# Performance work log

Measured on AMD Instinct MI355X. Metric: run time of the kernel, lower is better.

## Reference

```python
import jax, jax.numpy as jnp
import numpy as np
import math

D = 1024
H = 16
B = 4
N = 2048


def setup_inputs() -> dict:
    key = jax.random.key(0)
    ks = jax.random.split(key, 10)
    scale_qkv = 0.01
    def kaiming_uniform(k, shape, scale):
        # attenuated_kaiming_uniform_: fan_in = shape[1], gain for leaky_relu a=sqrt(5)
        fan_in = shape[1]
        gain = math.sqrt(2.0 / (1 + 5.0))
        bound = math.sqrt(3.0) * gain * scale / math.sqrt(fan_in)
        return jax.random.uniform(k, shape, jnp.float32, -bound, bound)
    return {
        "x_q": jax.random.normal(ks[0], (B, N, D), jnp.float32),
        "x_kv": jax.random.normal(ks[1], (B, N, D), jnp.float32),
        "Wq": kaiming_uniform(ks[2], (D, D), scale_qkv),
        "bq": jnp.zeros((D,), jnp.float32),
        "Wk": kaiming_uniform(ks[3], (D, D), scale_qkv),
        "bk": jnp.zeros((D,), jnp.float32),
        "Wv": kaiming_uniform(ks[4], (D, D), scale_qkv),
        "bv": jnp.zeros((D,), jnp.float32),
        "Wo": kaiming_uniform(ks[5], (D, D), 1.0),
        "bo": jnp.zeros((D,), jnp.float32),
    }


def reference(x_q, x_kv, Wq, bq, Wk, bk, Wv, bv, Wo, bo):
    bs, n, d = x_q.shape
    hd = d // H  # head dim
    # torch Linear: y = x @ W^T + b
    q = x_q @ Wq.T + bq
    k = x_kv @ Wk.T + bk
    v = x_kv @ Wv.T + bv
    # reshape to [bs, H, n, hd]
    q = q.reshape(bs, n, H, hd).transpose(0, 2, 1, 3)
    k = k.reshape(bs, n, H, hd).transpose(0, 2, 1, 3)
    v = v.reshape(bs, n, H, hd).transpose(0, 2, 1, 3)
    scores = jnp.einsum("bhqd,bhkd->bhqk", q, k) / math.sqrt(hd)
    seq_ids = jnp.arange(n)
    causal = (seq_ids[None, :] <= seq_ids[:, None]).astype(scores.dtype)  # [n, n]
    scores = scores + (1.0 - causal) * -10000.0
    probs = jax.nn.softmax(scores, axis=-1)
    out = jnp.einsum("bhqk,bhkd->bhqd", probs, v)
    out = out.transpose(0, 2, 1, 3).reshape(bs, n, d)
    return out @ Wo.T + bo
```

## Files before the change

kernel.cpp:

```cpp
#include <hip/hip_runtime.h>

typedef unsigned short u16;
typedef unsigned int u32;
typedef __attribute__((ext_vector_type(8))) short short8;
typedef __attribute__((ext_vector_type(4))) float f32x4;

#define ASYNC_CP16(gsrc, ldst) \
  __builtin_amdgcn_global_load_lds((__attribute__((address_space(1))) void*)(gsrc), \
                                   (__attribute__((address_space(3))) void*)(ldst), 16, 0, 0)

static __device__ __forceinline__ u16 f2bf(float f) {
  u32 u = __builtin_bit_cast(u32, f);
  u = u + 0x7fffu + ((u >> 16) & 1u);
  return (u16)(u >> 16);
}
static __device__ __forceinline__ u32 pk2(float a, float b) {
  return (u32)f2bf(a) | ((u32)f2bf(b) << 16);
}
static __device__ __forceinline__ u32 pk2r(float a, float b) {
  u32 ua = __builtin_bit_cast(u32, a) + 0x8000u;
  u32 ub = __builtin_bit_cast(u32, b) + 0x8000u;
  return __builtin_amdgcn_perm(ub, ua, 0x07060302);
}

__global__ __launch_bounds__(256) void convert_all(
    const float* __restrict__ xq, const float* __restrict__ xkv,
    const float* __restrict__ wq, const float* __restrict__ wk,
    const float* __restrict__ wv, const float* __restrict__ wo,
    u16* __restrict__ dst)
{
  long i = ((long)blockIdx.x * 256 + threadIdx.x) * 4;
  const float* s; long o;
  if      (i < 8388608)  { s = xq;  o = i; }
  else if (i < 16777216) { s = xkv; o = i - 8388608; }
  else if (i < 17825792) { s = wq;  o = i - 16777216; }
  else if (i < 18874368) { s = wk;  o = i - 17825792; }
  else if (i < 19922944) { s = wv;  o = i - 18874368; }
  else                   { s = wo;  o = i - 19922944; }
  float4 v = *(const float4*)(s + o);
  uint2 pkv; pkv.x = pk2(v.x, v.y); pkv.y = pk2(v.z, v.w);
  *(uint2*)(dst + i) = pkv;
}

template<int EPI>
__global__ __launch_bounds__(256)
void gemm_k(const u16* __restrict__ Axq, const u16* __restrict__ Axkv,
            const u16* __restrict__ W0, const u16* __restrict__ W1, const u16* __restrict__ W2,
            const float* __restrict__ b0, const float* __restrict__ b1, const float* __restrict__ b2,
            u16* __restrict__ Qo, u16* __restrict__ Ko, u16* __restrict__ Vo,
            float* __restrict__ Fo)
{
  __shared__ u16 lsa[128*32];
  __shared__ u16 lsb[128*32];
  const int tid = threadIdx.x;
  const int w = tid >> 6, lane = tid & 63;
  const int wr = w >> 1, wc = w & 1;
  const int bm = blockIdx.x, bn = blockIdx.y, z = blockIdx.z;
  const int l15 = lane & 15, l4 = lane >> 4;

  const u16* A; const u16* W; const float* bias;
  if (EPI == 0) {
    A    = (z == 0) ? Axq : Axkv;
    W    = (z == 0) ? W0 : (z == 1) ? W1 : W2;
    bias = (z == 0) ? b0 : (z == 1) ? b1 : b2;
  } else {
    A = Axq; W = W0; bias = b0;
  }
  const u16* Ag = A + (long)bm*128*1024;
  const u16* Wg = W + (long)bn*128*1024;

  f32x4 acc[4][4];
#pragma unroll
  for (int i = 0; i < 4; ++i)
#pragma unroll
    for (int j = 0; j < 4; ++j)
      acc[i][j] = (f32x4){0.f,0.f,0.f,0.f};

  for (int k0 = 0; k0 < 1024; k0 += 32) {
    __syncthreads();
#pragma unroll
    for (int c = 0; c < 2; ++c) {
      int tp = c*256 + tid;
      int row = tp >> 2, col = (tp & 3) * 8;
      ASYNC_CP16(Ag + (long)row*1024 + k0 + col, &lsa[tp*8]);
      ASYNC_CP16(Wg + (long)row*1024 + k0 + col, &lsb[tp*8]);
    }
    __syncthreads();
    short8 af[4], bfr[4];
#pragma unroll
    for (int i = 0; i < 4; ++i)
      af[i] = *(const short8*)&lsa[(wr*64 + i*16 + l15)*32 + l4*8];
#pragma unroll
    for (int j = 0; j < 4; ++j)
      bfr[j] = *(const short8*)&lsb[(wc*64 + j*16 + l15)*32 + l4*8];
#pragma unroll
    for (int i = 0; i < 4; ++i)
#pragma unroll
      for (int j = 0; j < 4; ++j)
        acc[i][j] = __builtin_amdgcn_mfma_f32_16x16x32_bf16(af[i], bfr[j], acc[i][j], 0, 0, 0);
  }

#pragma unroll
  for (int j = 0; j < 4; ++j) {
    const int colg = bn*128 + wc*64 + j*16 + l15;
    const float bb = bias[colg];
#pragma unroll
    for (int i = 0; i < 4; ++i) {
      const int rowg = bm*128 + wr*64 + i*16 + l4*4;
      if (EPI == 1) {
#pragma unroll
        for (int r = 0; r < 4; ++r)
          Fo[(long)(rowg + r)*1024 + colg] = acc[i][j][r] + bb;
      } else {
        const int b  = rowg >> 11, n0 = rowg & 2047;
        const int h  = colg >> 6,  c  = colg & 63;
        const int bh = b*16 + h;
        const long hb = (long)bh*131072 + (long)(n0 >> 7)*8192;
        if (z == 0) {
#pragma unroll
          for (int r = 0; r < 4; ++r)
            Qo[((long)bh*2048 + n0 + r)*64 + c] = f2bf((acc[i][j][r] + bb) * 0.18033688f);
        } else if (z == 1) {
          const long base = hb + (long)(c >> 3)*1024 + (n0 & 127)*8 + (c & 7);
#pragma unroll
          for (int r = 0; r < 4; ++r)
            Ko[base + r*8] = f2bf(acc[i][j][r] + bb);
        } else {
          const long base = hb + (long)((n0 & 127) >> 3)*512 + (long)c*8 + (n0 & 7);
          uint2 pkv;
          pkv.x = pk2(acc[i][j][0] + bb, acc[i][j][1] + bb);
          pkv.y = pk2(acc[i][j][2] + bb, acc[i][j][3] + bb);
          *(uint2*)(Vo + base) = pkv;
        }
      }
    }
  }
}

__global__ __launch_bounds__(256)
void attn_k(const u16* __restrict__ Q, const u16* __restrict__ K,
            const u16* __restrict__ V, u16* __restrict__ AO)
{
  __shared__ u16 lk[8192];
  __shared__ u16 lv[8192];
  __shared__ u16 lp[4][1024];
  const int tid = threadIdx.x;
  const int w = tid >> 6, lane = tid & 63;
  const int l15 = lane & 15, l4 = lane >> 4;
  const int qt = (gridDim.x - 1) - blockIdx.x;
  const int bh = blockIdx.y;
  const int q0 = qt*64;
  const int qg = q0 + w*16 + l15;
  const u16* Qh = Q + (long)bh*131072;
  const u16* Kh = K + (long)bh*131072;
  const u16* Vh = V + (long)bh*131072;

  short8 qf[2];
#pragma unroll
  for (int ks = 0; ks < 2; ++ks)
    qf[ks] = *(const short8*)&Qh[(long)qg*64 + ks*32 + l4*8];

  f32x4 o[4];
#pragma unroll
  for (int nt = 0; nt < 4; ++nt) o[nt] = (f32x4){0.f,0.f,0.f,0.f};
  float rsum = 0.f;

  u16* pw = &lp[w][0];
  const int swz_q = (l15 & 7);
  const int ktmax = (q0 + 63) >> 7;
  for (int kt = 0; kt <= ktmax; ++kt) {
    __syncthreads();
#pragma unroll
    for (int c = 0; c < 4; ++c) {
      int tp = c*256 + tid;
      ASYNC_CP16(Kh + (long)kt*8192 + tp*8, &lk[tp*8]);
      ASYNC_CP16(Vh + (long)kt*8192 + tp*8, &lv[tp*8]);
    }
    __syncthreads();

    f32x4 s[8];
#pragma unroll
    for (int nt = 0; nt < 8; ++nt) s[nt] = (f32x4){0.f,0.f,0.f,0.f};
#pragma unroll
    for (int ks = 0; ks < 2; ++ks)
#pragma unroll
      for (int nt = 0; nt < 8; ++nt) {
        short8 kf = *(const short8*)&lk[(ks*4 + l4)*1024 + (nt*16 + l15)*8];
        s[nt] = __builtin_amdgcn_mfma_f32_16x16x32_bf16(kf, qf[ks], s[nt], 0, 0, 0);
      }

    if (kt*128 + 127 > q0) {
      const int kb = kt*128 + l4*4;
#pragma unroll
      for (int nt = 0; nt < 8; ++nt)
#pragma unroll
        for (int r = 0; r < 4; ++r)
          if (kb + nt*16 + r > qg) s[nt][r] = -1e30f;
    }

    u32 pk[8][2];
#pragma unroll
    for (int nt = 0; nt < 8; ++nt) {
      float p0 = __builtin_amdgcn_exp2f(s[nt][0]);
      float p1 = __builtin_amdgcn_exp2f(s[nt][1]);
      float p2 = __builtin_amdgcn_exp2f(s[nt][2]);
      float p3 = __builtin_amdgcn_exp2f(s[nt][3]);
      rsum += (p0 + p1) + (p2 + p3);
      pk[nt][0] = pk2r(p0, p1);
      pk[nt][1] = pk2r(p2, p3);
    }

#pragma unroll
    for (int h = 0; h < 2; ++h) {
#pragma unroll
      for (int ntl = 0; ntl < 4; ++ntl) {
        const int chunk = ntl*2 + (l4 >> 1);
        const int swz = chunk ^ swz_q;
        uint2 pr; pr.x = pk[4*h + ntl][0]; pr.y = pk[4*h + ntl][1];
        *(uint2*)&pw[l15*64 + swz*8 + (l4 & 1)*4] = pr;
      }
#pragma unroll
      for (int ksl = 0; ksl < 2; ++ksl) {
        const int swz = (ksl*4 + l4) ^ swz_q;
        short8 pf = *(const short8*)&pw[l15*64 + swz*8];
        const int ksg = h*2 + ksl;
#pragma unroll
        for (int nt = 0; nt < 4; ++nt) {
          short8 vf = *(const short8*)&lv[(ksg*4 + l4)*512 + (nt*16 + l15)*8];
          o[nt] = __builtin_amdgcn_mfma_f32_16x16x32_bf16(vf, pf, o[nt], 0, 0, 0);
        }
      }
    }
  }

  rsum += __shfl_xor(rsum, 16, 64);
  rsum += __shfl_xor(rsum, 32, 64);

  const int b = bh >> 4, h = bh & 15;
  const float inv = 1.0f / rsum;
  const long tok = (long)b*2048 + qg;
#pragma unroll
  for (int nt = 0; nt < 4; ++nt) {
    uint2 pkv;
    pkv.x = pk2(o[nt][0]*inv, o[nt][1]*inv);
    pkv.y = pk2(o[nt][2]*inv, o[nt][3]*inv);
    *(uint2*)&AO[tok*1024 + h*64 + nt*16 + l4*4] = pkv;
  }
}

extern "C" void kernel_launch(void* const* d_in, const int* in_sizes, int n_in,
                              void* d_out, int out_size, void* d_ws, size_t ws_size,
                              hipStream_t stream)
{
  const float* xq  = (const float*)d_in[0];
  const float* xkv = (const float*)d_in[1];
  const float* Wq  = (const float*)d_in[2];
  const float* bq  = (const float*)d_in[3];
  const float* Wk  = (const float*)d_in[4];
  const float* bk  = (const float*)d_in[5];
  const float* Wv  = (const float*)d_in[6];
  const float* bv  = (const float*)d_in[7];
  const float* Wo  = (const float*)d_in[8];
  const float* bo  = (const float*)d_in[9];

  u16* ws    = (u16*)d_ws;
  u16* xq_b  = ws;
  u16* xkv_b = xq_b  + (1l<<23);
  u16* wq_b  = xkv_b + (1l<<23);
  u16* wk_b  = wq_b  + (1l<<20);
  u16* wv_b  = wk_b  + (1l<<20);
  u16* wo_b  = wv_b  + (1l<<20);
  u16* Qb    = wo_b  + (1l<<20);
  u16* Kb    = Qb    + (1l<<23);
  u16* Vb    = Kb    + (1l<<23);
  u16* Ab    = Vb    + (1l<<23);

  convert_all<<<20480, 256, 0, stream>>>(xq, xkv, Wq, Wk, Wv, Wo, ws);
  gemm_k<0><<<dim3(64,8,3), 256, 0, stream>>>(xq_b, xkv_b, wq_b, wk_b, wv_b,
                                              bq, bk, bv, Qb, Kb, Vb, nullptr);
  attn_k<<<dim3(32,64), 256, 0, stream>>>(Qb, Kb, Vb, Ab);
  gemm_k<1><<<dim3(64,8,1), 256, 0, stream>>>(Ab, nullptr, wo_b, nullptr, nullptr,
                                              bo, nullptr, nullptr,
                                              nullptr, nullptr, nullptr,
                                              (float*)d_out);
}
```

Baseline: 344.1 us.

## Enlarge attention query tiles, keep P in registers, skip masked diagonal tiles

The attention kernel now processes 128 queries per block (32 per wave, two 16-row groups), so each K/V tile loaded into LDS is reused twice as much and the grid halves. The P matrix no longer round-trips through LDS: exp values stay in registers and feed 16x16x16 bf16 MFMAs with V as the A operand, which needs a new swizzled V layout written by the projection GEMM. The last (diagonal) tile is specialised to skip fully masked sub-tiles. The GEMM epilogue swaps operands for Q/K/output so stores become vectorised along the feature dimension. The cost is more registers per wave, and it relies on the MFMA16 builtin choice being correct.

Result: slower. 406.4 us (+18.1%).

```diff
diff --git a/kernel.cpp b/kernel.cpp
--- a/kernel.cpp
+++ b/kernel.cpp
@@ -3,11 +3,24 @@
 typedef unsigned short u16;
 typedef unsigned int u32;
 typedef __attribute__((ext_vector_type(8))) short short8;
+typedef __attribute__((ext_vector_type(4))) short s16x4;
 typedef __attribute__((ext_vector_type(4))) float f32x4;
 
 #define ASYNC_CP16(gsrc, ldst) \
   __builtin_amdgcn_global_load_lds((__attribute__((address_space(1))) void*)(gsrc), \
                                    (__attribute__((address_space(3))) void*)(ldst), 16, 0, 0)
+
+#if __has_builtin(__builtin_amdgcn_mfma_f32_16x16x16bf16_1k)
+#define MFMA16(A, B, C) __builtin_amdgcn_mfma_f32_16x16x16bf16_1k(A, B, C, 0, 0, 0)
+#elif __has_builtin(__builtin_amdgcn_mfma_f32_16x16x16_bf16)
+#define MFMA16(A, B, C) __builtin_amdgcn_mfma_f32_16x16x16_bf16(A, B, C, 0, 0, 0)
+#else
+static __device__ __forceinline__ f32x4 mfma16_asm(s16x4 a, s16x4 b, f32x4 c) {
+  asm("v_mfma_f32_16x16x16_bf16 %0, %1, %2, %0" : "+v"(c) : "v"(a), "v"(b));
+  return c;
+}
+#define MFMA16(A, B, C) mfma16_asm(A, B, C)
+#endif
 
 static __device__ __forceinline__ u16 f2bf(float f) {
   u32 u = __builtin_bit_cast(u32, f);
@@ -69,6 +82,10 @@
   const u16* Ag = A + (long)bm*128*1024;
   const u16* Wg = W + (long)bn*128*1024;
 
+  const bool swapop = (EPI == 1) || (z != 2);
+  const u16* pAs = swapop ? lsb : lsa;
+  const u16* pBs = swapop ? lsa : lsb;
+
   f32x4 acc[4][4];
 #pragma unroll
   for (int i = 0; i < 4; ++i)
@@ -89,10 +106,10 @@
     short8 af[4], bfr[4];
 #pragma unroll
     for (int i = 0; i < 4; ++i)
-      af[i] = *(const short8*)&lsa[(wr*64 + i*16 + l15)*32 + l4*8];
+      af[i] = *(const short8*)&pAs[(wr*64 + i*16 + l15)*32 + l4*8];
 #pragma unroll
     for (int j = 0; j < 4; ++j)
-      bfr[j] = *(const short8*)&lsb[(wc*64 + j*16 + l15)*32 + l4*8];
+      bfr[j] = *(const short8*)&pBs[(wc*64 + j*16 + l15)*32 + l4*8];
 #pragma unroll
     for (int i = 0; i < 4; ++i)
 #pragma unroll
@@ -100,37 +117,122 @@
         acc[i][j] = __builtin_amdgcn_mfma_f32_16x16x32_bf16(af[i], bfr[j], acc[i][j], 0, 0, 0);
   }
 
-#pragma unroll
-  for (int j = 0; j < 4; ++j) {
-    const int colg = bn*128 + wc*64 + j*16 + l15;
-    const float bb = bias[colg];
+  if (swapop) {
 #pragma unroll
     for (int i = 0; i < 4; ++i) {
-      const int rowg = bm*128 + wr*64 + i*16 + l4*4;
-      if (EPI == 1) {
-#pragma unroll
-        for (int r = 0; r < 4; ++r)
-          Fo[(long)(rowg + r)*1024 + colg] = acc[i][j][r] + bb;
-      } else {
-        const int b  = rowg >> 11, n0 = rowg & 2047;
-        const int h  = colg >> 6,  c  = colg & 63;
-        const int bh = b*16 + h;
-        const long hb = (long)bh*131072 + (long)(n0 >> 7)*8192;
-        if (z == 0) {
-#pragma unroll
-          for (int r = 0; r < 4; ++r)
-            Qo[((long)bh*2048 + n0 + r)*64 + c] = f2bf((acc[i][j][r] + bb) * 0.18033688f);
-        } else if (z == 1) {
-          const long base = hb + (long)(c >> 3)*1024 + (n0 & 127)*8 + (c & 7);
-#pragma unroll
-          for (int r = 0; r < 4; ++r)
-            Ko[base + r*8] = f2bf(acc[i][j][r] + bb);
+      const int dg = bn*128 + wr*64 + i*16 + l4*4;
+      const float4 b4 = *(const float4*)&bias[dg];
+#pragma unroll
+      for (int j = 0; j < 4; ++j) {
+        const int tk = bm*128 + wc*64 + j*16 + l15;
+        const float v0 = acc[i][j][0] + b4.x, v1 = acc[i][j][1] + b4.y;
+        const float v2 = acc[i][j][2] + b4.z, v3 = acc[i][j][3] + b4.w;
+        if (EPI == 1) {
+          *(float4*)&Fo[(long)tk*1024 + dg] = (float4){v0, v1, v2, v3};
+        } else if (z == 0) {
+          const int bb_ = tk >> 11, n = tk & 2047, h = dg >> 6, c0 = dg & 63;
+          uint2 pv;
+          pv.x = pk2(v0*0.18033688f, v1*0.18033688f);
+          pv.y = pk2(v2*0.18033688f, v3*0.18033688f);
+          *(uint2*)&Qo[((long)(bb_*16 + h)*2048 + n)*64 + c0] = pv;
         } else {
-          const long base = hb + (long)((n0 & 127) >> 3)*512 + (long)c*8 + (n0 & 7);
-          uint2 pkv;
-          pkv.x = pk2(acc[i][j][0] + bb, acc[i][j][1] + bb);
-          pkv.y = pk2(acc[i][j][2] + bb, acc[i][j][3] + bb);
-          *(uint2*)(Vo + base) = pkv;
+          const int bb_ = tk >> 11, n = tk & 2047, h = dg >> 6, d0 = dg & 63;
+          const long base = (long)(bb_*16 + h)*131072 + (long)(n >> 7)*8192
+                          + (d0 >> 3)*1024 + (n & 127)*8 + (d0 & 7);
+          uint2 pv; pv.x = pk2(v0, v1); pv.y = pk2(v2, v3);
+          *(uint2*)&Ko[base] = pv;
+        }
+      }
+    }
+  } else {
+#pragma unroll
+    for (int j = 0; j < 4; ++j) {
+      const int colg = bn*128 + wc*64 + j*16 + l15;
+      const float bb = bias[colg];
+      const int h = colg >> 6, c = colg & 63;
+#pragma unroll
+      for (int i = 0; i < 4; ++i) {
+        const int rowg = bm*128 + wr*64 + i*16 + l4*4;
+        const int bb_ = rowg >> 11, n0 = rowg & 2047;
+        const long base = (long)(bb_*16 + h)*131072 + (long)(n0 >> 7)*8192
+                        + ((n0 & 127) >> 5)*2048 + (long)c*32
+                        + ((n0 >> 4) & 1)*4 + ((((n0 >> 2) & 3) ^ ((c >> 1) & 3)))*8;
+        uint2 pv;
+        pv.x = pk2(acc[i][j][0] + bb, acc[i][j][1] + bb);
+        pv.y = pk2(acc[i][j][2] + bb, acc[i][j][3] + bb);
+        *(uint2*)&Vo[base] = pv;
+      }
+    }
+  }
+}
+
+template<bool LAST>
+static __device__ __forceinline__ void attn_step(
+    const u16* __restrict__ Kh, const u16* __restrict__ Vh, long kt,
+    u16* lk, u16* lv, int tid, int w, int l4, int l15,
+    const short8 (&qf)[2][2], f32x4 (&o)[2][4], float (&rs)[2])
+{
+  __syncthreads();
+#pragma unroll
+  for (int c2 = 0; c2 < 4; ++c2) {
+    int tp = c2*256 + tid;
+    ASYNC_CP16(Kh + kt*8192 + tp*8, &lk[tp*8]);
+    ASYNC_CP16(Vh + kt*8192 + tp*8, &lv[tp*8]);
+  }
+  __syncthreads();
+
+  s16x4 pkv[2][8];
+#pragma unroll
+  for (int c = 0; c < 2; ++c) {
+    const int ntl = 2*w + c;
+    f32x4 s[8];
+#pragma unroll
+    for (int nt = 0; nt < 8; ++nt) {
+      if (!LAST || nt <= ntl) {
+        f32x4 a = (f32x4){0.f,0.f,0.f,0.f};
+#pragma unroll
+        for (int ks = 0; ks < 2; ++ks) {
+          short8 kf = *(const short8*)&lk[(ks*4 + l4)*1024 + (nt*16 + l15)*8];
+          a = __builtin_amdgcn_mfma_f32_16x16x32_bf16(kf, qf[c][ks], a, 0, 0, 0);
+        }
+        s[nt] = a;
+      }
+    }
+    if (LAST) {
+#pragma unroll
+      for (int r = 0; r < 4; ++r)
+        if (l4*4 + r > l15) s[ntl][r] = -1e30f;
+    }
+#pragma unroll
+    for (int nt = 0; nt < 8; ++nt) {
+      if (!LAST || nt <= ntl) {
+        float p0 = __builtin_amdgcn_exp2f(s[nt][0]);
+        float p1 = __builtin_amdgcn_exp2f(s[nt][1]);
+        float p2 = __builtin_amdgcn_exp2f(s[nt][2]);
+        float p3 = __builtin_amdgcn_exp2f(s[nt][3]);
+        rs[c] += (p0 + p1) + (p2 + p3);
+        union { uint2 u; s16x4 v; } pu;
+        pu.u.x = pk2r(p0, p1);
+        pu.u.y = pk2r(p2, p3);
+        pkv[c][nt] = pu.v;
+      }
+    }
+  }
+
+  const int swz = l4 ^ ((l15 >> 1) & 3);
+#pragma unroll
+  for (int g = 0; g < 4; ++g) {
+    if (!LAST || 2*g <= 2*w + 1) {
+#pragma unroll
+      for (int ntd = 0; ntd < 4; ++ntd) {
+        short8 vv = *(const short8*)&lv[g*2048 + (ntd*16 + l15)*32 + swz*8];
+        s16x4 v0 = __builtin_shufflevector(vv, vv, 0, 1, 2, 3);
+        s16x4 v1 = __builtin_shufflevector(vv, vv, 4, 5, 6, 7);
+#pragma unroll
+        for (int c = 0; c < 2; ++c) {
+          const int ntl = 2*w + c;
+          if (!LAST || 2*g <= ntl)     o[c][ntd] = MFMA16(v0, pkv[c][2*g],     o[c][ntd]);
+          if (!LAST || 2*g + 1 <= ntl) o[c][ntd] = MFMA16(v1, pkv[c][2*g + 1], o[c][ntd]);
         }
       }
     }
@@ -143,108 +245,49 @@
 {
   __shared__ u16 lk[8192];
   __shared__ u16 lv[8192];
-  __shared__ u16 lp[4][1024];
   const int tid = threadIdx.x;
   const int w = tid >> 6, lane = tid & 63;
   const int l15 = lane & 15, l4 = lane >> 4;
-  const int qt = (gridDim.x - 1) - blockIdx.x;
+  const int qt = 15 - blockIdx.x;
   const int bh = blockIdx.y;
-  const int q0 = qt*64;
-  const int qg = q0 + w*16 + l15;
+  const int q0 = qt*128, qbase = q0 + w*32;
   const u16* Qh = Q + (long)bh*131072;
   const u16* Kh = K + (long)bh*131072;
   const u16* Vh = V + (long)bh*131072;
 
-  short8 qf[2];
-#pragma unroll
-  for (int ks = 0; ks < 2; ++ks)
-    qf[ks] = *(const short8*)&Qh[(long)qg*64 + ks*32 + l4*8];
-
-  f32x4 o[4];
-#pragma unroll
-  for (int nt = 0; nt < 4; ++nt) o[nt] = (f32x4){0.f,0.f,0.f,0.f};
-  float rsum = 0.f;
-
-  u16* pw = &lp[w][0];
-  const int swz_q = (l15 & 7);
-  const int ktmax = (q0 + 63) >> 7;
-  for (int kt = 0; kt <= ktmax; ++kt) {
-    __syncthreads();
-#pragma unroll
-    for (int c = 0; c < 4; ++c) {
-      int tp = c*256 + tid;
-      ASYNC_CP16(Kh + (long)kt*8192 + tp*8, &lk[tp*8]);
-      ASYNC_CP16(Vh + (long)kt*8192 + tp*8, &lv[tp*8]);
-    }
-    __syncthreads();
-
-    f32x4 s[8];
-#pragma unroll
-    for (int nt = 0; nt < 8; ++nt) s[nt] = (f32x4){0.f,0.f,0.f,0.f};
+  short8 qf[2][2];
+#pragma unroll
+  for (int c = 0; c < 2; ++c)
 #pragma unroll
     for (int ks = 0; ks < 2; ++ks)
-#pragma unroll
-      for (int nt = 0; nt < 8; ++nt) {
-        short8 kf = *(const short8*)&lk[(ks*4 + l4)*1024 + (nt*16 + l15)*8];
-        s[nt] = __builtin_amdgcn_mfma_f32_16x16x32_bf16(kf, qf[ks], s[nt], 0, 0, 0);
-      }
-
-    if (kt*128 + 127 > q0) {
-      const int kb = kt*128 + l4*4;
-#pragma unroll
-      for (int nt = 0; nt < 8; ++nt)
-#pragma unroll
-        for (int r = 0; r < 4; ++r)
-          if (kb + nt*16 + r > qg) s[nt][r] = -1e30f;
-    }
-
-    u32 pk[8][2];
-#pragma unroll
-    for (int nt = 0; nt < 8; ++nt) {
-      float p0 = __builtin_amdgcn_exp2f(s[nt][0]);
-      float p1 = __builtin_amdgcn_exp2f(s[nt][1]);
-      float p2 = __builtin_amdgcn_exp2f(s[nt][2]);
-      float p3 = __builtin_amdgcn_exp2f(s[nt][3]);
-      rsum += (p0 + p1) + (p2 + p3);
-      pk[nt][0] = pk2r(p0, p1);
-      pk[nt][1] = pk2r(p2, p3);
-    }
-
-#pragma unroll
-    for (int h = 0; h < 2; ++h) {
-#pragma unroll
-      for (int ntl = 0; ntl < 4; ++ntl) {
-        const int chunk = ntl*2 + (l4 >> 1);
-        const int swz = chunk ^ swz_q;
-        uint2 pr; pr.x = pk[4*h + ntl][0]; pr.y = pk[4*h + ntl][1];
-        *(uint2*)&pw[l15*64 + swz*8 + (l4 & 1)*4] = pr;
-      }
-#pragma unroll
-      for (int ksl = 0; ksl < 2; ++ksl) {
-        const int swz = (ksl*4 + l4) ^ swz_q;
-        short8 pf = *(const short8*)&pw[l15*64 + swz*8];
-        const int ksg = h*2 + ksl;
-#pragma unroll
-        for (int nt = 0; nt < 4; ++nt) {
-          short8 vf = *(const short8*)&lv[(ksg*4 + l4)*512 + (nt*16 + l15)*8];
-          o[nt] = __builtin_amdgcn_mfma_f32_16x16x32_bf16(vf, pf, o[nt], 0, 0, 0);
-        }
-      }
-    }
-  }
-
-  rsum += __shfl_xor(rsum, 16, 64);
-  rsum += __shfl_xor(rsum, 32, 64);
+      qf[c][ks] = *(const short8*)&Qh[(long)(qbase + c*16 + l15)*64 + ks*32 + l4*8];
+
+  f32x4 o[2][4];
+#pragma unroll
+  for (int c = 0; c < 2; ++c)
+#pragma unroll
+    for (int nt = 0; nt < 4; ++nt) o[c][nt] = (f32x4){0.f,0.f,0.f,0.f};
+  float rs[2] = {0.f, 0.f};
+
+  for (int kt = 0; kt < qt; ++kt)
+    attn_step<false>(Kh, Vh, kt, lk, lv, tid, w, l4, l15, qf, o, rs);
+  attn_step<true>(Kh, Vh, qt, lk, lv, tid, w, l4, l15, qf, o, rs);
 
   const int b = bh >> 4, h = bh & 15;
-  const float inv = 1.0f / rsum;
-  const long tok = (long)b*2048 + qg;
-#pragma unroll
-  for (int nt = 0; nt < 4; ++nt) {
-    uint2 pkv;
-    pkv.x = pk2(o[nt][0]*inv, o[nt][1]*inv);
-    pkv.y = pk2(o[nt][2]*inv, o[nt][3]*inv);
-    *(uint2*)&AO[tok*1024 + h*64 + nt*16 + l4*4] = pkv;
+#pragma unroll
+  for (int c = 0; c < 2; ++c) {
+    float t = rs[c];
+    t += __shfl_xor(t, 16, 64);
+    t += __shfl_xor(t, 32, 64);
+    const float inv = 1.0f / t;
+    const long tok = (long)b*2048 + qbase + c*16 + l15;
+#pragma unroll
+    for (int ntd = 0; ntd < 4; ++ntd) {
+      uint2 pv;
+      pv.x = pk2(o[c][ntd][0]*inv, o[c][ntd][1]*inv);
+      pv.y = pk2(o[c][ntd][2]*inv, o[c][ntd][3]*inv);
+      *(uint2*)&AO[tok*1024 + h*64 + ntd*16 + l4*4] = pv;
+    }
   }
 }
 
@@ -278,7 +321,7 @@
   convert_all<<<20480, 256, 0, stream>>>(xq, xkv, Wq, Wk, Wv, Wo, ws);
   gemm_k<0><<<dim3(64,8,3), 256, 0, stream>>>(xq_b, xkv_b, wq_b, wk_b, wv_b,
                                               bq, bk, bv, Qb, Kb, Vb, nullptr);
-  attn_k<<<dim3(32,64), 256, 0, stream>>>(Qb, Kb, Vb, Ab);
+  attn_k<<<dim3(16,64), 256, 0, stream>>>(Qb, Kb, Vb, Ab);
   gemm_k<1><<<dim3(64,8,1), 256, 0, stream>>>(Ab, nullptr, wo_b, nullptr, nullptr,
                                               bo, nullptr, nullptr,
                                               nullptr, nullptr, nullptr,
```
